# Optimization experiments

Hardware: AMD Instinct MI355X
Metric: run time of the kernel (lower is better)

## Reference

```python
import jax, jax.numpy as jnp
import numpy as np

B, L, D = 8, 512, 256


def hard_sigmoid(x):
    # Keras 1.x default inner_activation for LSTM gates
    return jnp.clip(0.2 * x + 0.5, 0.0, 1.0)


def lstm_step(x_t, h, c, W, U, b):
    # gates in Keras order: i, f, g(candidate), o
    z = x_t @ W + h @ U + b  # (B, 4D)
    i, f, g, o = jnp.split(z, 4, axis=-1)
    i = hard_sigmoid(i)
    f = hard_sigmoid(f)
    g = jnp.tanh(g)
    o = hard_sigmoid(o)
    c_new = f * c + i * g
    h_new = o * jnp.tanh(c_new)
    return h_new, c_new


def setup_inputs() -> dict:
    key = jax.random.key(0)
    ks = jax.random.split(key, 10)
    s = 1.0 / np.sqrt(D)
    x = jax.random.normal(ks[0], (B, L, D), dtype=jnp.float32)
    W_r = jax.random.normal(ks[1], (D, 4 * D), dtype=jnp.float32) * s
    U_r = jax.random.normal(ks[2], (D, 4 * D), dtype=jnp.float32) * s
    b_r = jnp.zeros((4 * D,), dtype=jnp.float32)
    W_w = jax.random.normal(ks[3], (D, 4 * D), dtype=jnp.float32) * s
    U_w = jax.random.normal(ks[4], (D, 4 * D), dtype=jnp.float32) * s
    b_w = jnp.zeros((4 * D,), dtype=jnp.float32)
    W_c = jax.random.normal(ks[5], (2 * D, D), dtype=jnp.float32) * s
    b_c = jnp.zeros((D,), dtype=jnp.float32)
    return {"x": x, "W_r": W_r, "U_r": U_r, "b_r": b_r,
            "W_w": W_w, "U_w": U_w, "b_w": b_w, "W_c": W_c, "b_c": b_c}


def reference(x, W_r, U_r, b_r, W_w, U_w, b_w, W_c, b_c):
    Bb, Ll, Dd = x.shape
    h0 = jnp.zeros((Bb, Dd), dtype=x.dtype)

    # --- reader LSTM (return_sequences=True), eq. 1 ---
    def reader_step(carry, x_t):
        h, c = carry
        h, c = lstm_step(x_t, h, c, W_r, U_r, b_r)
        return (h, c), h

    _, o_seq = jax.lax.scan(reader_step, (h0, h0), jnp.swapaxes(x, 0, 1))  # (L, B, D)

    # --- compose-and-write loop, eqs. 2-6; mem_0 = x ---
    def write_step(carry, o_t):
        mem, h, c = carry  # mem: (B, L, D)
        z = jax.nn.softmax(jnp.einsum('bd,bld->bl', o_t, mem), axis=-1)  # (B, L)
        m_rt = jnp.einsum('bl,bld->bd', z, mem)                           # (B, D)
        c_t = jnp.concatenate([o_t, m_rt], axis=-1) @ W_c + b_c          # linear composer
        h_new, c_new = lstm_step(c_t, h, c, W_w, U_w, b_w)
        mem_new = mem * (1.0 - z[..., None]) + h_new[:, None, :] * z[..., None]
        return (mem_new, h_new, c_new), h_new

    (_, _, _), h_seq = jax.lax.scan(write_step, (x, h0, h0), o_seq)
    # return_mode == 'last_output'
    return h_seq[-1]
```

## Files before the change

kernel.cpp:

```cpp
#include <hip/hip_runtime.h>
#include <math.h>

#define BB 8
#define LL 512
#define DD 256
#define NG4 1024
#define WGB 32
#define WR 16
#define WU 8
#define MLD 264

typedef __attribute__((ext_vector_type(4))) float f32x4;

static const size_t OFF_XW    = 0;
static const size_t OFF_F     = OFF_XW + (size_t)BB*LL*NG4;
static const size_t OFF_BMW   = OFF_F + (size_t)DD*NG4;
static const size_t OFF_B2    = OFF_BMW + (size_t)DD*NG4;
static const size_t OFF_HR    = OFF_B2 + NG4;
static const size_t OFF_HW    = OFF_HR + (size_t)2*BB*DD;
static const size_t OFF_PMAX  = OFF_HW + (size_t)BB*DD;
static const size_t OFF_PSUM  = OFF_PMAX + (size_t)BB*WGB;
static const size_t OFF_RHO   = OFF_PSUM + (size_t)BB*WGB;
static const size_t OFF_PM    = OFF_RHO + (size_t)BB*WGB;
static const size_t OFF_FLAGS = OFF_PM + (size_t)BB*WGB*DD;
static const size_t TOTAL_WS  = OFF_FLAGS + BB*32;

__device__ __forceinline__ float hsig(float x) {
    return fminf(fmaxf(0.2f*x + 0.5f, 0.0f), 1.0f);
}

__device__ __forceinline__ void st_coh(float* p, float v) {
    __hip_atomic_store(p, v, __ATOMIC_RELAXED, __HIP_MEMORY_SCOPE_AGENT);
}
__device__ __forceinline__ float ld_coh(const float* p) {
    return __hip_atomic_load(p, __ATOMIC_RELAXED, __HIP_MEMORY_SCOPE_AGENT);
}
__device__ __forceinline__ unsigned ld_coh_u(const unsigned* p) {
    return __hip_atomic_load(p, __ATOMIC_RELAXED, __HIP_MEMORY_SCOPE_AGENT);
}

__device__ __forceinline__ void ld_pm8(
    const f32x4* p0, const f32x4* p1, const f32x4* p2, const f32x4* p3,
    const f32x4* p4, const f32x4* p5, const f32x4* p6, const f32x4* p7,
    f32x4& a0, f32x4& a1, f32x4& a2, f32x4& a3,
    f32x4& a4, f32x4& a5, f32x4& a6, f32x4& a7)
{
    asm volatile(
        "global_load_dwordx4 %0, %8, off sc0 sc1\n\t"
        "global_load_dwordx4 %1, %9, off sc0 sc1\n\t"
        "global_load_dwordx4 %2, %10, off sc0 sc1\n\t"
        "global_load_dwordx4 %3, %11, off sc0 sc1\n\t"
        "global_load_dwordx4 %4, %12, off sc0 sc1\n\t"
        "global_load_dwordx4 %5, %13, off sc0 sc1\n\t"
        "global_load_dwordx4 %6, %14, off sc0 sc1\n\t"
        "global_load_dwordx4 %7, %15, off sc0 sc1\n\t"
        "s_waitcnt vmcnt(0)"
        : "=&v"(a0), "=&v"(a1), "=&v"(a2), "=&v"(a3),
          "=&v"(a4), "=&v"(a5), "=&v"(a6), "=&v"(a7)
        : "v"(p0), "v"(p1), "v"(p2), "v"(p3),
          "v"(p4), "v"(p5), "v"(p6), "v"(p7)
        : "memory");
}

template<int TM, int TN, int TK>
__global__ void __launch_bounds__(256) gemm_nn(
    const float* __restrict__ A, int lda,
    const float* __restrict__ Bmat, int ldb,
    const float* __restrict__ bias,
    float* __restrict__ C, int ldc,
    int M, int N, int K)
{
    __shared__ float As[TK][TM];
    __shared__ float Bs[TK][TN];
    const int m0 = blockIdx.y * TM, n0 = blockIdx.x * TN;
    const int tid = threadIdx.x;
    const int tx = tid % (TN/4);
    const int ty = tid / (TN/4);
    float acc[4][4] = {};
    for (int k0 = 0; k0 < K; k0 += TK) {
        {
            const int e = tid*4;
            const int m = e / TK, k = e % TK;
            const float4 v = *reinterpret_cast<const float4*>(&A[(size_t)(m0+m)*lda + k0 + k]);
            As[k+0][m] = v.x; As[k+1][m] = v.y; As[k+2][m] = v.z; As[k+3][m] = v.w;
        }
        {
            const int e = tid*4;
            const int k = e / TN, n = e % TN;
            const float4 v = *reinterpret_cast<const float4*>(&Bmat[(size_t)(k0+k)*ldb + n0 + n]);
            Bs[k][n+0] = v.x; Bs[k][n+1] = v.y; Bs[k][n+2] = v.z; Bs[k][n+3] = v.w;
        }
        __syncthreads();
        #pragma unroll
        for (int kk = 0; kk < TK; ++kk) {
            float a[4], bv[4];
            #pragma unroll
            for (int i = 0; i < 4; ++i) a[i] = As[kk][ty*4+i];
            #pragma unroll
            for (int j = 0; j < 4; ++j) bv[j] = Bs[kk][tx*4+j];
            #pragma unroll
            for (int i = 0; i < 4; ++i)
                #pragma unroll
                for (int j = 0; j < 4; ++j) acc[i][j] += a[i]*bv[j];
        }
        __syncthreads();
    }
    #pragma unroll
    for (int i = 0; i < 4; ++i) {
        const int m = m0 + ty*4 + i;
        #pragma unroll
        for (int j = 0; j < 4; ++j) {
            const int n = n0 + tx*4 + j;
            C[(size_t)m*ldc + n] = acc[i][j] + (bias ? bias[n] : 0.0f);
        }
    }
}

__global__ void __launch_bounds__(256) b2_kernel(
    const float* __restrict__ bc, const float* __restrict__ Ww,
    const float* __restrict__ bw, float* __restrict__ B2)
{
    const int n = blockIdx.x*256 + threadIdx.x;
    float a = bw[n];
    for (int k = 0; k < DD; ++k) a += bc[k]*Ww[(size_t)k*NG4 + n];
    B2[n] = a;
}

__global__ void __launch_bounds__(256) fused_kernel(
    const float* __restrict__ XW, const float* __restrict__ Fw,
    const float* __restrict__ Bm, const float* __restrict__ B2,
    const float* __restrict__ Ur, const float* __restrict__ Uw,
    const float* __restrict__ x,
    float* __restrict__ HR, float* __restrict__ HWb,
    float* __restrict__ PMAX, float* __restrict__ PSUM, float* __restrict__ RHO,
    float* __restrict__ PM,
    unsigned* __restrict__ flags, float* __restrict__ out)
{
    extern __shared__ float sm[];
    float* Urs  = sm;
    float* Uws  = Urs + 8192;
    float* Fs   = Uws + 8192;
    float* Bms  = Fs + 8192;
    float* mems = Bms + 8192;
    float* hr2  = mems + WR*MLD;
    float* hw   = hr2 + 512;
    float* ms   = hw + 256;
    float* zredR= ms + 256;
    float* zredW= zredR + 256;
    float* red4 = zredW + 256;
    float* xws  = red4 + 1024;
    float* b2s  = xws + 32;
    float* zrs  = b2s + 32;
    float* zws  = zrs + 32;
    float* fwS  = zws + 32;
    float* d1   = fwS + 32;
    float* zp   = d1 + 16;
    float* esx  = zp + 16;
    float* wv   = esx + 16;
    float* cr   = wv + 16;
    float* cw   = cr + 8;
    float* misc = cw + 8;

    const int b   = (int)blockIdx.x & 7;
    const int wg  = (int)blockIdx.x >> 3;
    const int tid = threadIdx.x;
    const int R0  = wg*WR;
    const int U0  = wg*WU;
    const int gc32 = (tid>>3)*DD + U0 + (tid&7);

    for (int it = 0; it < 32; ++it) {
        const int e = it*256 + tid;
        const int k = e >> 5, cl = e & 31;
        const int gc = (cl>>3)*DD + U0 + (cl&7);
        Urs[k*32+cl] = Ur[(size_t)k*NG4 + gc];
        Uws[k*32+cl] = Uw[(size_t)k*NG4 + gc];
        Fs [k*32+cl] = Fw[(size_t)k*NG4 + gc];
        Bms[k*32+cl] = Bm[(size_t)k*NG4 + gc];
    }
    if (tid < 32) b2s[tid] = B2[gc32];
    for (int r = 0; r < WR; ++r)
        mems[r*MLD + tid] = x[((size_t)b*LL + R0 + r)*DD + tid];
    {
        const size_t base = (size_t)b*LL*NG4;
        const float zi = XW[base + tid];
        const float zg = XW[base + 512 + tid];
        const float zo = XW[base + 768 + tid];
        const float c0 = hsig(zi)*tanhf(zg);
        hr2[tid] = hsig(zo)*tanhf(c0);
        hr2[256 + tid] = 0.f;
        if (tid >= U0 && tid < U0+WU) cr[tid-U0] = c0;
    }
    if (tid < 16) { zp[tid] = 0.f; d1[tid] = 0.f; esx[tid] = 0.f; }
    if (tid < 8)  cw[tid] = 0.f;
    if (tid < 4)  misc[tid] = 0.f;
    __syncthreads();

    unsigned* flb = &flags[b*32];

    for (int s = 0; s <= LL; ++s) {
        const bool doW = (s >= 1);
        float* hrN_s = hr2 + (s&1)*256;
        float* hrO_s = hr2 + ((s+1)&1)*256;

        float xw_r = 0.f;
        if (s <= LL-2 && tid < 32) xw_r = XW[((size_t)b*LL + s + 1)*NG4 + gc32];
        float hw_r = 0.f, rho_r = 0.f;
        if (s >= 2) {
            hw_r = ld_coh(&HWb[b*DD + tid]);
            if (tid < 32) rho_r = ld_coh(&RHO[b*WGB + tid]);
        }
        hw[tid] = hw_r;

        if (tid < 32) {
            float d2 = rho_r;
            #pragma unroll
            for (int off = 16; off; off >>= 1) d2 += __shfl_xor(d2, off, 32);
            if (doW && tid < 16) {
                const float zpv = zp[tid];
                const float sc  = (1.f - zpv)*d1[tid] + zpv*d2;
                float m = sc;
                #pragma unroll
                for (int off = 8; off; off >>= 1) m = fmaxf(m, __shfl_xor(m, off, 16));
                const float e = __expf(sc - m);
                esx[tid] = e;
                wv[tid]  = e*(1.f - zpv);
                float sum = e, bp = e*zpv;
                #pragma unroll
                for (int off = 8; off; off >>= 1) {
                    sum += __shfl_xor(sum, off, 16);
                    bp  += __shfl_xor(bp,  off, 16);
                }
                if (tid == 0) {
                    misc[2] = bp;
                    st_coh(&PMAX[b*WGB + wg], m);
                    st_coh(&PSUM[b*WGB + wg], sum);
                }
            }
        }
        __syncthreads();

        if (doW) {
            float p = misc[2]*hw_r;
            #pragma unroll
            for (int r = 0; r < WR; ++r) p += wv[r]*mems[r*MLD + tid];
            st_coh(&PM[((size_t)b*WGB + wg)*DD + tid], p);
        }

        asm volatile("s_waitcnt vmcnt(0)" ::: "memory");
        __syncthreads();
        if (tid == 0)
            __hip_atomic_fetch_add(flb, 1u, __ATOMIC_RELAXED, __HIP_MEMORY_SCOPE_AGENT);
        if (s >= 2) {
            #pragma unroll
            for (int r = 0; r < WR; ++r) {
                const float z = zp[r];
                float* mp = &mems[r*MLD + tid];
                *mp = *mp*(1.f - z) + hw_r*z;
            }
        }
        if (doW) {
            const int kc = tid >> 5, cl = tid & 31, k0 = kc*32;
            float a = 0.f;
            #pragma unroll 8
            for (int k = k0; k < k0+32; ++k)
                a += hw[k]*Uws[k*32+cl] + hrO_s[k]*Fs[k*32+cl];
            zredW[tid] = a;
        }
        if (tid == 0) {
            const unsigned target = 64u*(unsigned)s + 32u;
            while (ld_coh_u(flb) < target) __builtin_amdgcn_s_sleep(1);
        }
        __syncthreads();

        float hrN_r = 0.f;
        if (s >= 1 && s <= LL-1) hrN_r = ld_coh(&HR[((size_t)(s&1))*BB*DD + b*DD + tid]);
        float pmx_r = 0.f, ps_r = 0.f;
        if (doW && tid < 32) {
            pmx_r = ld_coh(&PMAX[b*WGB + tid]);
            ps_r  = ld_coh(&PSUM[b*WGB + tid]);
        }
        f32x4 a0,a1,a2,a3,a4,a5,a6,a7;
        const int w0 = tid >> 6, dq = tid & 63;
        if (doW) {
            const float* pmb = PM + (size_t)b*WGB*DD;
            ld_pm8((const f32x4*)(pmb + (w0+ 0)*DD) + dq, (const f32x4*)(pmb + (w0+ 4)*DD) + dq,
                   (const f32x4*)(pmb + (w0+ 8)*DD) + dq, (const f32x4*)(pmb + (w0+12)*DD) + dq,
                   (const f32x4*)(pmb + (w0+16)*DD) + dq, (const f32x4*)(pmb + (w0+20)*DD) + dq,
                   (const f32x4*)(pmb + (w0+24)*DD) + dq, (const f32x4*)(pmb + (w0+28)*DD) + dq,
                   a0,a1,a2,a3,a4,a5,a6,a7);
        }
        if (s >= 1 && s <= LL-1) hrN_s[tid] = hrN_r;
        if (s <= LL-2 && tid < 32) xws[tid] = xw_r;
        __syncthreads();

        if (doW && tid < 32) {
            float g = pmx_r;
            #pragma unroll
            for (int off = 16; off; off >>= 1) g = fmaxf(g, __shfl_xor(g, off, 32));
            const float fw = __expf(pmx_r - g);
            float S = ps_r*fw;
            #pragma unroll
            for (int off = 16; off; off >>= 1) S += __shfl_xor(S, off, 32);
            fwS[tid] = fw;
            if (tid == 0)  misc[1] = 1.f/S;
            if (tid == wg) misc[0] = fw/S;
        }
        if (s <= LL-2) {
            const int kc = tid >> 5, cl = tid & 31, k0 = kc*32;
            float a = 0.f;
            #pragma unroll 8
            for (int k = k0; k < k0+32; ++k) a += hrN_s[k]*Urs[k*32+cl];
            zredR[tid] = a;
        }
        __syncthreads();

        if (doW) {
            f32x4 acc = a0*fwS[w0];
            acc += a1*fwS[w0+4];  acc += a2*fwS[w0+8];
            acc += a3*fwS[w0+12]; acc += a4*fwS[w0+16];
            acc += a5*fwS[w0+20]; acc += a6*fwS[w0+24];
            acc += a7*fwS[w0+28];
            *(f32x4*)(red4 + w0*DD + dq*4) = acc;
        }
        __syncthreads();
        if (doW) {
            ms[tid] = (red4[tid] + red4[DD+tid] + red4[2*DD+tid] + red4[3*DD+tid]) * misc[1];
            if (tid < 16) zp[tid] = esx[tid]*misc[0];
        }
        __syncthreads();
        if (doW) {
            const int kc = tid >> 5, cl = tid & 31, k0 = kc*32;
            float a = zredW[tid];
            #pragma unroll 8
            for (int k = k0; k < k0+32; ++k) a += ms[k]*Bms[k*32+cl];
            zredW[tid] = a;
        }
        __syncthreads();
        if (tid < 32) {
            if (doW) {
                float z = b2s[tid];
                #pragma unroll
                for (int q = 0; q < 8; ++q) z += zredW[q*32 + tid];
                zws[tid] = z;
            }
            if (s <= LL-2) {
                float z = xws[tid];
                #pragma unroll
                for (int q = 0; q < 8; ++q) z += zredR[q*32 + tid];
                zrs[tid] = z;
            }
        }
        __syncthreads();

        if (doW && tid < 8) {
            const float ig = hsig(zws[tid]);
            const float fg = hsig(zws[8+tid]);
            const float gg = tanhf(zws[16+tid]);
            const float og = hsig(zws[24+tid]);
            const float c  = fg*cw[tid] + ig*gg;
            cw[tid] = c;
            const float h = og*tanhf(c);
            st_coh(&HWb[b*DD + U0 + tid], h);
            if (s < LL) {
                float rr = h * hrN_s[U0 + tid];
                rr += __shfl_down(rr, 4, 8);
                rr += __shfl_down(rr, 2, 8);
                rr += __shfl_down(rr, 1, 8);
                if (tid == 0) st_coh(&RHO[b*WGB + wg], rr);
            }
            if (s == LL) out[b*DD + U0 + tid] = h;
        }
        if (s <= LL-2 && tid < 8) {
            const float ig = hsig(zrs[tid]);
            const float fg = hsig(zrs[8+tid]);
            const float gg = tanhf(zrs[16+tid]);
            const float og = hsig(zrs[24+tid]);
            const float c  = fg*cr[tid] + ig*gg;
            cr[tid] = c;
            st_coh(&HR[((size_t)((s+1)&1))*BB*DD + b*DD + U0 + tid], og*tanhf(c));
        }

        if (s < LL) {
            asm volatile("s_waitcnt vmcnt(0)" ::: "memory");
            __syncthreads();
            if (tid == 0)
                __hip_atomic_fetch_add(flb, 1u, __ATOMIC_RELAXED, __HIP_MEMORY_SCOPE_AGENT);
            {
                const int r = tid >> 4, j = tid & 15;
                float a = 0.f;
                const float* mrow = mems + r*MLD;
                #pragma unroll 4
                for (int d = j; d < DD; d += 16) a += hrN_s[d]*mrow[d];
                #pragma unroll
                for (int off = 8; off; off >>= 1) a += __shfl_down(a, off, 16);
                if (j == 0) d1[r] = a;
            }
            if (tid == 0) {
                const unsigned target = 64u*(unsigned)s + 64u;
                while (ld_coh_u(flb) < target) __builtin_amdgcn_s_sleep(1);
            }
            __syncthreads();
        }
    }
}

extern "C" void kernel_launch(void* const* d_in, const int* in_sizes, int n_in,
                              void* d_out, int out_size, void* d_ws, size_t ws_size,
                              hipStream_t stream) {
    const float* x   = (const float*)d_in[0];
    const float* W_r = (const float*)d_in[1];
    const float* U_r = (const float*)d_in[2];
    const float* b_r = (const float*)d_in[3];
    const float* W_w = (const float*)d_in[4];
    const float* U_w = (const float*)d_in[5];
    const float* b_w = (const float*)d_in[6];
    const float* W_c = (const float*)d_in[7];
    const float* b_c = (const float*)d_in[8];
    (void)in_sizes; (void)n_in;

    if (ws_size < TOTAL_WS * sizeof(float)) return;

    float* ws   = (float*)d_ws;
    float* XW   = ws + OFF_XW;
    float* Fmat = ws + OFF_F;
    float* Bmw  = ws + OFF_BMW;
    float* B2   = ws + OFF_B2;
    float* HR   = ws + OFF_HR;
    float* HWb  = ws + OFF_HW;
    float* PMAX = ws + OFF_PMAX;
    float* PSUM = ws + OFF_PSUM;
    float* RHO  = ws + OFF_RHO;
    float* PM   = ws + OFF_PM;
    unsigned* flags = (unsigned*)(ws + OFF_FLAGS);

    const int FUSED_LDS = 39800 * 4;
    hipFuncSetAttribute((const void*)fused_kernel, hipFuncAttributeMaxDynamicSharedMemorySize, FUSED_LDS);

    hipMemsetAsync(flags, 0, BB*32*sizeof(unsigned), stream);

    dim3 blk(256);
    gemm_nn<64,64,16><<<dim3(NG4/64, (BB*LL)/64), blk, 0, stream>>>(
        x, DD, W_r, NG4, b_r, XW, NG4, BB*LL, NG4, DD);
    gemm_nn<64,64,16><<<dim3(NG4/64, DD/64), blk, 0, stream>>>(
        W_c, DD, W_w, NG4, nullptr, Fmat, NG4, DD, NG4, DD);
    gemm_nn<64,64,16><<<dim3(NG4/64, DD/64), blk, 0, stream>>>(
        W_c + (size_t)DD*DD, DD, W_w, NG4, nullptr, Bmw, NG4, DD, NG4, DD);
    b2_kernel<<<dim3(NG4/256), blk, 0, stream>>>(b_c, W_w, b_w, B2);
    fused_kernel<<<dim3(BB*WGB), blk, FUSED_LDS, stream>>>(
        XW, Fmat, Bmw, B2, U_r, U_w, x, HR, HWb, PMAX, PSUM, RHO, PM, flags, (float*)d_out);
}
```

Before: 3.984 ms.

## Replace atomic counter barrier with per-workgroup flags polled by every wave

The inter-workgroup barrier no longer uses a single atomic counter that one thread sleep-polls. Each workgroup now stores its own monotonically increasing epoch flag, and every wave polls all 32 flags with vectorised coherent loads, with no s_sleep. This removes atomic contention on one address, the post-poll __syncthreads and the sleep latency. The local __syncthreads placement is reshuffled to fit, which adds one barrier earlier in the step, and busy-polling from every wave adds memory traffic.

Measured after the change: 3.947 ms. Within noise of the previous version (-0.9%).

```diff
diff --git a/kernel.cpp b/kernel.cpp
--- a/kernel.cpp
+++ b/kernel.cpp
@@ -11,6 +11,7 @@
 #define MLD 264
 
 typedef __attribute__((ext_vector_type(4))) float f32x4;
+typedef __attribute__((ext_vector_type(4))) unsigned u32x4;
 
 static const size_t OFF_XW    = 0;
 static const size_t OFF_F     = OFF_XW + (size_t)BB*LL*NG4;
@@ -23,7 +24,7 @@
 static const size_t OFF_RHO   = OFF_PSUM + (size_t)BB*WGB;
 static const size_t OFF_PM    = OFF_RHO + (size_t)BB*WGB;
 static const size_t OFF_FLAGS = OFF_PM + (size_t)BB*WGB*DD;
-static const size_t TOTAL_WS  = OFF_FLAGS + BB*32;
+static const size_t TOTAL_WS  = OFF_FLAGS + BB*WGB;
 
 __device__ __forceinline__ float hsig(float x) {
     return fminf(fmaxf(0.2f*x + 0.5f, 0.0f), 1.0f);
@@ -35,8 +36,26 @@
 __device__ __forceinline__ float ld_coh(const float* p) {
     return __hip_atomic_load(p, __ATOMIC_RELAXED, __HIP_MEMORY_SCOPE_AGENT);
 }
-__device__ __forceinline__ unsigned ld_coh_u(const unsigned* p) {
-    return __hip_atomic_load(p, __ATOMIC_RELAXED, __HIP_MEMORY_SCOPE_AGENT);
+__device__ __forceinline__ void st_coh_u(unsigned* p, unsigned v) {
+    __hip_atomic_store(p, v, __ATOMIC_RELAXED, __HIP_MEMORY_SCOPE_AGENT);
+}
+
+__device__ __forceinline__ u32x4 ld_coh_u4(const unsigned* p) {
+    u32x4 r;
+    asm volatile("global_load_dwordx4 %0, %1, off sc0 sc1\n\t"
+                 "s_waitcnt vmcnt(0)"
+                 : "=&v"(r) : "v"(p) : "memory");
+    return r;
+}
+
+__device__ __forceinline__ void wave_poll(const unsigned* flb, unsigned target, int tid) {
+    if ((tid & 63) < 8) {
+        const unsigned* fp = flb + (tid & 63)*4;
+        for (;;) {
+            u32x4 v = ld_coh_u4(fp);
+            if (v[0] >= target && v[1] >= target && v[2] >= target && v[3] >= target) break;
+        }
+    }
 }
 
 __device__ __forceinline__ void ld_pm8(
@@ -195,7 +214,7 @@
     if (tid < 4)  misc[tid] = 0.f;
     __syncthreads();
 
-    unsigned* flb = &flags[b*32];
+    unsigned* flb = &flags[b*WGB];
 
     for (int s = 0; s <= LL; ++s) {
         const bool doW = (s >= 1);
@@ -210,6 +229,9 @@
             if (tid < 32) rho_r = ld_coh(&RHO[b*WGB + tid]);
         }
         hw[tid] = hw_r;
+        __syncthreads();
+
+        if (s <= LL-2 && tid < 32) xws[tid] = xw_r;
 
         if (tid < 32) {
             float d2 = rho_r;
@@ -248,8 +270,8 @@
 
         asm volatile("s_waitcnt vmcnt(0)" ::: "memory");
         __syncthreads();
-        if (tid == 0)
-            __hip_atomic_fetch_add(flb, 1u, __ATOMIC_RELAXED, __HIP_MEMORY_SCOPE_AGENT);
+        const unsigned tgt1 = 2u*(unsigned)s + 1u;
+        if (tid == 0) st_coh_u(&flb[wg], tgt1);
         if (s >= 2) {
             #pragma unroll
             for (int r = 0; r < WR; ++r) {
@@ -266,11 +288,7 @@
                 a += hw[k]*Uws[k*32+cl] + hrO_s[k]*Fs[k*32+cl];
             zredW[tid] = a;
         }
-        if (tid == 0) {
-            const unsigned target = 64u*(unsigned)s + 32u;
-            while (ld_coh_u(flb) < target) __builtin_amdgcn_s_sleep(1);
-        }
-        __syncthreads();
+        wave_poll(flb, tgt1, tid);
 
         float hrN_r = 0.f;
         if (s >= 1 && s <= LL-1) hrN_r = ld_coh(&HR[((size_t)(s&1))*BB*DD + b*DD + tid]);
@@ -290,9 +308,6 @@
                    a0,a1,a2,a3,a4,a5,a6,a7);
         }
         if (s >= 1 && s <= LL-1) hrN_s[tid] = hrN_r;
-        if (s <= LL-2 && tid < 32) xws[tid] = xw_r;
-        __syncthreads();
-
         if (doW && tid < 32) {
             float g = pmx_r;
             #pragma unroll
@@ -305,6 +320,8 @@
             if (tid == 0)  misc[1] = 1.f/S;
             if (tid == wg) misc[0] = fw/S;
         }
+        __syncthreads();
+
         if (s <= LL-2) {
             const int kc = tid >> 5, cl = tid & 31, k0 = kc*32;
             float a = 0.f;
@@ -312,8 +329,6 @@
             for (int k = k0; k < k0+32; ++k) a += hrN_s[k]*Urs[k*32+cl];
             zredR[tid] = a;
         }
-        __syncthreads();
-
         if (doW) {
             f32x4 acc = a0*fwS[w0];
             acc += a1*fwS[w0+4];  acc += a2*fwS[w0+8];
@@ -383,8 +398,8 @@
         if (s < LL) {
             asm volatile("s_waitcnt vmcnt(0)" ::: "memory");
             __syncthreads();
-            if (tid == 0)
-                __hip_atomic_fetch_add(flb, 1u, __ATOMIC_RELAXED, __HIP_MEMORY_SCOPE_AGENT);
+            const unsigned tgt2 = 2u*(unsigned)s + 2u;
+            if (tid == 0) st_coh_u(&flb[wg], tgt2);
             {
                 const int r = tid >> 4, j = tid & 15;
                 float a = 0.f;
@@ -395,11 +410,7 @@
                 for (int off = 8; off; off >>= 1) a += __shfl_down(a, off, 16);
                 if (j == 0) d1[r] = a;
             }
-            if (tid == 0) {
-                const unsigned target = 64u*(unsigned)s + 64u;
-                while (ld_coh_u(flb) < target) __builtin_amdgcn_s_sleep(1);
-            }
-            __syncthreads();
+            wave_poll(flb, tgt2, tid);
         }
     }
 }
@@ -436,7 +447,7 @@
     const int FUSED_LDS = 39800 * 4;
     hipFuncSetAttribute((const void*)fused_kernel, hipFuncAttributeMaxDynamicSharedMemorySize, FUSED_LDS);
 
-    hipMemsetAsync(flags, 0, BB*32*sizeof(unsigned), stream);
+    hipMemsetAsync(flags, 0, BB*WGB*sizeof(unsigned), stream);
 
     dim3 blk(256);
     gemm_nn<64,64,16><<<dim3(NG4/64, (BB*LL)/64), blk, 0, stream>>>(
```
